# Performance work log

Measured on AMD Instinct MI355X. Metric: run time of the kernel, lower is better.

The kernel has to match this reference:

```python
import jax, jax.numpy as jnp
import numpy as np

B, S, C, K = 4, 4096, 2048, 4


def setup_inputs() -> dict:
    key = jax.random.key(0)
    k1, k2, k3 = jax.random.split(key, 3)
    hidden_states = jax.random.normal(k1, (B, S, C), dtype=jnp.float32)
    attention_mask = jnp.ones((B, S), dtype=jnp.float32)
    # depthwise conv weight: [out_channels, in_channels/groups=1, K]
    W = jax.random.normal(k2, (C, 1, K), dtype=jnp.float32) * 0.02
    b = jax.random.normal(k3, (C,), dtype=jnp.float32) * 0.02
    return {"hidden_states": hidden_states, "attention_mask": attention_mask, "W": W, "b": b}


def reference(hidden_states, attention_mask, W, b):
    # prefill path: input_state=None, return_cache_state=True,
    # conv1d_padding = K-1, stride = 1, activation = silu (depthwise causal conv)
    kernel_size = W.shape[-1]
    channels = W.shape[0]
    # mask padding tokens (B>1 and S>1 so the mask is applied)
    x = hidden_states * attention_mask[:, :, None]            # [B, S, C]
    xT = jnp.transpose(x, (0, 2, 1))                          # [B, C, S]
    # cache state: F.pad(xT, (K - S, 0)) with S > K trims to the last K steps
    input_state = xT[..., -kernel_size:]                      # [B, C, K]
    # causal depthwise conv: left-pad K-1 so output length == S and y[t] only sees x[<=t]
    y = jax.lax.conv_general_dilated(
        xT, W,
        window_strides=(1,),
        padding=[(kernel_size - 1, 0)],
        feature_group_count=channels,
        dimension_numbers=("NCH", "OIH", "NCH"),
    )                                                          # [B, C, S]
    y = y + b[None, :, None]
    y = jnp.transpose(y, (0, 2, 1))                            # [B, S, C]
    y = jax.nn.silu(y)
    y = y * attention_mask[:, :, None]
    return y, input_state
```

## Files before the change

kernel.cpp:

```cpp
#include <hip/hip_runtime.h>
#include <math.h>

#define BB 4
#define SS 4096
#define CC 2048
#define KK 4

constexpr int TS      = 64;
constexpr int THREADS = 256;
constexpr int CGRP    = THREADS * 4;
constexpr int CBLK    = CC / CGRP;
constexpr int SBLK    = SS / TS;

__device__ __forceinline__ float silu(float v) {
    return v / (1.0f + __expf(-v));
}

__global__ __launch_bounds__(THREADS) void causal_conv_kernel(
    const float* __restrict__ x,
    const float* __restrict__ mask,
    const float* __restrict__ W,
    const float* __restrict__ bias,
    float* __restrict__ y)
{
    const int blk = blockIdx.x;
    const int b   = blk / (CBLK * SBLK);
    const int r   = blk % (CBLK * SBLK);
    const int cb  = r % CBLK;
    const int s0  = (r / CBLK) * TS;
    const int c   = cb * CGRP + threadIdx.x * 4;

    const float4 w0 = *(const float4*)(W + (size_t)(c + 0) * KK);
    const float4 w1 = *(const float4*)(W + (size_t)(c + 1) * KK);
    const float4 w2 = *(const float4*)(W + (size_t)(c + 2) * KK);
    const float4 w3 = *(const float4*)(W + (size_t)(c + 3) * KK);
    const float4 bv = *(const float4*)(bias + c);

    const float* xb = x + (size_t)b * SS * CC + c;
    float*       yb = y + (size_t)b * SS * CC + c;
    const float* mb = mask + (size_t)b * SS;

    float4 xm3, xm2, xm1;
    {
        #define LOADX(sv, dst)                                              \
            if ((sv) < 0) { dst = make_float4(0.f, 0.f, 0.f, 0.f); }        \
            else {                                                          \
                float m_ = mb[(sv)];                                        \
                float4 v_ = *(const float4*)(xb + (size_t)(sv) * CC);       \
                dst = make_float4(v_.x * m_, v_.y * m_, v_.z * m_, v_.w * m_); \
            }
        LOADX(s0 - 3, xm3)
        LOADX(s0 - 2, xm2)
        LOADX(s0 - 1, xm1)
        #undef LOADX
    }

    #pragma unroll 4
    for (int s = s0; s < s0 + TS; ++s) {
        const float m = mb[s];
        float4 xc = *(const float4*)(xb + (size_t)s * CC);
        xc.x *= m; xc.y *= m; xc.z *= m; xc.w *= m;

        float4 acc;
        acc.x = fmaf(w0.x, xm3.x, fmaf(w0.y, xm2.x, fmaf(w0.z, xm1.x, fmaf(w0.w, xc.x, bv.x))));
        acc.y = fmaf(w1.x, xm3.y, fmaf(w1.y, xm2.y, fmaf(w1.z, xm1.y, fmaf(w1.w, xc.y, bv.y))));
        acc.z = fmaf(w2.x, xm3.z, fmaf(w2.y, xm2.z, fmaf(w2.z, xm1.z, fmaf(w2.w, xc.z, bv.z))));
        acc.w = fmaf(w3.x, xm3.w, fmaf(w3.y, xm2.w, fmaf(w3.z, xm1.w, fmaf(w3.w, xc.w, bv.w))));

        float4 outv;
        outv.x = silu(acc.x) * m;
        outv.y = silu(acc.y) * m;
        outv.z = silu(acc.z) * m;
        outv.w = silu(acc.w) * m;

        *(float4*)(yb + (size_t)s * CC) = outv;

        xm3 = xm2; xm2 = xm1; xm1 = xc;
    }
}

__global__ __launch_bounds__(256) void state_kernel(
    const float* __restrict__ x,
    const float* __restrict__ mask,
    float* __restrict__ state)
{
    const int idx = blockIdx.x * blockDim.x + threadIdx.x;
    if (idx >= BB * CC) return;
    const int b = idx / CC;
    const int c = idx % CC;
    const float* xb = x + (size_t)b * SS * CC + c;
    const float* mb = mask + (size_t)b * SS;

    float4 st;
    st.x = xb[(size_t)(SS - 4) * CC] * mb[SS - 4];
    st.y = xb[(size_t)(SS - 3) * CC] * mb[SS - 3];
    st.z = xb[(size_t)(SS - 2) * CC] * mb[SS - 2];
    st.w = xb[(size_t)(SS - 1) * CC] * mb[SS - 1];

    *(float4*)(state + (size_t)idx * 4) = st;
}

extern "C" void kernel_launch(void* const* d_in, const int* in_sizes, int n_in,
                              void* d_out, int out_size, void* d_ws, size_t ws_size,
                              hipStream_t stream) {
    const float* x    = (const float*)d_in[0];
    const float* mask = (const float*)d_in[1];
    const float* W    = (const float*)d_in[2];
    const float* bias = (const float*)d_in[3];

    float* y     = (float*)d_out;
    float* state = y + (size_t)BB * SS * CC;

    causal_conv_kernel<<<BB * CBLK * SBLK, THREADS, 0, stream>>>(x, mask, W, bias, y);
    state_kernel<<<(BB * CC + 255) / 256, 256, 0, stream>>>(x, mask, state);
}
```

Before: 51.94 us.

## Fuse cache-state write into conv kernel, shrink sequence tile, use nontemporal stores

Drops the separate state kernel: the last sequence tile now writes the final K masked inputs from its register history, which saves one launch and a re-read of x. The sequence tile is cut from 64 to 16 to get more blocks, with a launch-bounds occupancy hint. Output stores become nontemporal to avoid polluting cache. The smaller tile raises the share of halo reloads per block.

Measured after the change: 50.47 us. 2.8% less time.

```diff
diff --git a/kernel.cpp b/kernel.cpp
--- a/kernel.cpp
+++ b/kernel.cpp
@@ -6,22 +6,25 @@
 #define CC 2048
 #define KK 4
 
-constexpr int TS      = 64;
+constexpr int TS      = 16;
 constexpr int THREADS = 256;
 constexpr int CGRP    = THREADS * 4;
 constexpr int CBLK    = CC / CGRP;
 constexpr int SBLK    = SS / TS;
 
+typedef float floatx4 __attribute__((ext_vector_type(4)));
+
 __device__ __forceinline__ float silu(float v) {
     return v / (1.0f + __expf(-v));
 }
 
-__global__ __launch_bounds__(THREADS) void causal_conv_kernel(
+__global__ __launch_bounds__(THREADS, 8) void causal_conv_kernel(
     const float* __restrict__ x,
     const float* __restrict__ mask,
     const float* __restrict__ W,
     const float* __restrict__ bias,
-    float* __restrict__ y)
+    float* __restrict__ y,
+    float* __restrict__ state)
 {
     const int blk = blockIdx.x;
     const int b   = blk / (CBLK * SBLK);
@@ -40,7 +43,7 @@
     float*       yb = y + (size_t)b * SS * CC + c;
     const float* mb = mask + (size_t)b * SS;
 
-    float4 xm3, xm2, xm1;
+    float4 xm4, xm3, xm2, xm1;
     {
         #define LOADX(sv, dst)                                              \
             if ((sv) < 0) { dst = make_float4(0.f, 0.f, 0.f, 0.f); }        \
@@ -67,37 +70,24 @@
         acc.z = fmaf(w2.x, xm3.z, fmaf(w2.y, xm2.z, fmaf(w2.z, xm1.z, fmaf(w2.w, xc.z, bv.z))));
         acc.w = fmaf(w3.x, xm3.w, fmaf(w3.y, xm2.w, fmaf(w3.z, xm1.w, fmaf(w3.w, xc.w, bv.w))));
 
-        float4 outv;
+        floatx4 outv;
         outv.x = silu(acc.x) * m;
         outv.y = silu(acc.y) * m;
         outv.z = silu(acc.z) * m;
         outv.w = silu(acc.w) * m;
 
-        *(float4*)(yb + (size_t)s * CC) = outv;
+        __builtin_nontemporal_store(outv, (floatx4*)(yb + (size_t)s * CC));
 
-        xm3 = xm2; xm2 = xm1; xm1 = xc;
+        xm4 = xm3; xm3 = xm2; xm2 = xm1; xm1 = xc;
     }
-}
 
-__global__ __launch_bounds__(256) void state_kernel(
-    const float* __restrict__ x,
-    const float* __restrict__ mask,
-    float* __restrict__ state)
-{
-    const int idx = blockIdx.x * blockDim.x + threadIdx.x;
-    if (idx >= BB * CC) return;
-    const int b = idx / CC;
-    const int c = idx % CC;
-    const float* xb = x + (size_t)b * SS * CC + c;
-    const float* mb = mask + (size_t)b * SS;
-
-    float4 st;
-    st.x = xb[(size_t)(SS - 4) * CC] * mb[SS - 4];
-    st.y = xb[(size_t)(SS - 3) * CC] * mb[SS - 3];
-    st.z = xb[(size_t)(SS - 2) * CC] * mb[SS - 2];
-    st.w = xb[(size_t)(SS - 1) * CC] * mb[SS - 1];
-
-    *(float4*)(state + (size_t)idx * 4) = st;
+    if (s0 == SS - TS) {
+        float* st = state + ((size_t)b * CC + c) * KK;
+        *(float4*)(st + 0)  = make_float4(xm4.x, xm3.x, xm2.x, xm1.x);
+        *(float4*)(st + 4)  = make_float4(xm4.y, xm3.y, xm2.y, xm1.y);
+        *(float4*)(st + 8)  = make_float4(xm4.z, xm3.z, xm2.z, xm1.z);
+        *(float4*)(st + 12) = make_float4(xm4.w, xm3.w, xm2.w, xm1.w);
+    }
 }
 
 extern "C" void kernel_launch(void* const* d_in, const int* in_sizes, int n_in,
@@ -111,6 +101,5 @@
     float* y     = (float*)d_out;
     float* state = y + (size_t)BB * SS * CC;
 
-    causal_conv_kernel<<<BB * CBLK * SBLK, THREADS, 0, stream>>>(x, mask, W, bias, y);
-    state_kernel<<<(BB * CC + 255) / 256, 256, 0, stream>>>(x, mask, state);
+    causal_conv_kernel<<<BB * CBLK * SBLK, THREADS, 0, stream>>>(x, mask, W, bias, y, state);
 }
```
